# Kernel optimization log

Measured on AMD Instinct MI355X. Metric: run time of the kernel, lower is better.

The kernel has to match this reference:

```python
import jax, jax.numpy as jnp
import numpy as np

W_SIZE = 7
K = 15
EPS = 1e-8  # torch cosine_similarity eps


def setup_inputs() -> dict:
    key = jax.random.key(0)
    k0, k1, k2 = jax.random.split(key, 3)
    dim = 128
    return {
        "x_in": jax.random.normal(k0, (4, dim, 112, 112), dtype=jnp.float32),
        "f_w": jax.random.normal(k1, (dim // 8, dim), dtype=jnp.float32) * (1.0 / np.sqrt(dim)),
        "f_b": jax.random.normal(k2, (dim // 8,), dtype=jnp.float32) * 0.01,
        "edge_alpha": jnp.ones((1,), dtype=jnp.float32),
        "edge_beta": jnp.zeros((1,), dtype=jnp.float32),
    }


def reference(x_in, f_w, f_b, edge_alpha, edge_beta):
    B, C, H, W = x_in.shape
    Wg = Hg = W_SIZE
    w, h = H // Wg, W // Hg
    N = w * h
    # patchify: b c (Wg w) (Hg h) -> (b Wg Hg) c w h
    xp = x_in.reshape(B, C, Wg, w, Hg, h).transpose(0, 2, 4, 1, 3, 5).reshape(B * Wg * Hg, C, w, h)
    P = xp.shape[0]
    # 1x1 conv f: C -> C//8 channels
    f = jnp.einsum('pcwh,dc->pdwh', xp, f_w) + f_b[None, :, None, None]
    Cf = f.shape[1]
    x_flat = f.reshape(P, Cf, N).transpose(0, 2, 1)  # [P, N, Cf]
    # normalized spatial grid (torch std is unbiased -> ddof=1)
    gi, gj = jnp.meshgrid(jnp.arange(w, dtype=jnp.float32), jnp.arange(h, dtype=jnp.float32), indexing='ij')
    grid = jnp.stack([gi, gj], axis=-1).reshape(N, 2)
    grid = (grid - grid.mean(0)) / (grid.std(0, ddof=1) + 1e-5)
    x_aug = jnp.concatenate([x_flat, jnp.broadcast_to(grid[None], (P, N, 2))], axis=-1)  # [P,N,Cf+2]
    # pairwise cosine similarity via normalized dot products
    nrm = jnp.maximum(jnp.linalg.norm(x_aug, axis=-1, keepdims=True), EPS)
    xn = x_aug / nrm
    sim = jnp.einsum('pnd,pmd->pnm', xn, xn)  # [P,N,N]
    topv, topi = jax.lax.top_k(sim, K)        # [P,N,K]
    # edge weights; scatter_softmax over row index == softmax over k (each row has exactly K edges)
    weights = jax.nn.sigmoid(edge_beta[0] + edge_alpha[0] * topv)
    wn = jax.nn.softmax(weights, axis=-1)     # [P,N,K]
    # gather original-channel messages from top-k neighbors and aggregate
    xo = xp.reshape(P, C, N).transpose(0, 2, 1)                 # [P,N,C]
    gathered = jax.vmap(lambda xr, ir: xr[ir])(xo, topi)        # [P,N,K,C]
    out_flat = jnp.einsum('pnk,pnkc->pnc', wn, gathered)        # [P,N,C]
    out = out_flat.reshape(P, w, h, C).transpose(0, 3, 1, 2)    # [P,C,w,h]
    # un-patchify: (b Wg Hg) c w h -> b c (Wg w) (Hg h)
    out = out.reshape(B, Wg, Hg, C, w, h).transpose(0, 3, 1, 4, 2, 5).reshape(B, C, H, W)
    return out
```

## Files before the change

kernel.cpp:

```cpp
#include <hip/hip_runtime.h>
#include <math.h>

#define KSEL 15
#define CIN 128
#define CF 16
#define HH 112
#define PLANE 12544
#define NN 256
#define GRIDW 7
#define ROWSTRIDE 20

static __device__ __forceinline__ unsigned mono32(float f) {
    unsigned u = __float_as_uint(f);
    return ((int)u < 0) ? ~u : (u | 0x80000000u);
}
static __device__ __forceinline__ float demono32(unsigned u) {
    return ((int)u < 0) ? __uint_as_float(u & 0x7FFFFFFFu) : __uint_as_float(~u);
}
static __device__ __forceinline__ unsigned long long mono64(double f) {
    unsigned long long u = (unsigned long long)__double_as_longlong(f);
    return ((long long)u < 0) ? ~u : (u | 0x8000000000000000ull);
}

__global__ __launch_bounds__(256) void k1_features(
    const float* __restrict__ x, const float* __restrict__ fw, const float* __restrict__ fb,
    double* __restrict__ xa64, float* __restrict__ xa32)
{
    __shared__ float lfw[CIN * CF];
    __shared__ float lfb[CF];
    const int tid = threadIdx.x;
    const int p  = blockIdx.x >> 2;
    const int n0 = (blockIdx.x & 3) * 64;
    const int b = p / 49, g = p % 49;
    const int gI = g / 7, gJ = g % 7;
    const float* xb = x + (size_t)b * CIN * PLANE + (size_t)(gI * 16 * HH + gJ * 16);

    for (int q = tid; q < CIN * CF; q += 256) { int d = q >> 7, c = q & 127; lfw[c * CF + d] = fw[q]; }
    if (tid < CF) lfb[tid] = fb[tid];
    __syncthreads();

    const int nl = tid >> 2, dq = tid & 3;
    const int n = n0 + nl, i = n >> 4, j = n & 15;
    const float* xp = xb + i * HH + j;

    double a0 = 0.0, a1 = 0.0, a2 = 0.0, a3 = 0.0;
#pragma unroll 4
    for (int c = 0; c < CIN; ++c) {
        double xc = (double)xp[(size_t)c * PLANE];
        float4 wv = *(const float4*)&lfw[c * CF + dq * 4];
        a0 = fma(xc, (double)wv.x, a0);
        a1 = fma(xc, (double)wv.y, a1);
        a2 = fma(xc, (double)wv.z, a2);
        a3 = fma(xc, (double)wv.w, a3);
    }
    a0 += (double)lfb[dq * 4 + 0];
    a1 += (double)lfb[dq * 4 + 1];
    a2 += (double)lfb[dq * 4 + 2];
    a3 += (double)lfb[dq * 4 + 3];

    const double GDIV = 4.618802153517006 + 1e-5;
    double gx = ((double)i - 7.5) / GDIV;
    double gy = ((double)j - 7.5) / GDIV;

    double ss = a0 * a0;
    ss = fma(a1, a1, ss); ss = fma(a2, a2, ss); ss = fma(a3, a3, ss);
    if (dq == 3) { ss = fma(gx, gx, ss); ss = fma(gy, gy, ss); }
    ss += __shfl_xor(ss, 1);
    ss += __shfl_xor(ss, 2);
    double nrm = fmax(sqrt(ss), 1e-8);

    size_t ro = ((size_t)p * NN + n) * ROWSTRIDE;
    double o0 = a0 / nrm, o1 = a1 / nrm, o2 = a2 / nrm, o3 = a3 / nrm;
    xa64[ro + dq * 4 + 0] = o0; xa64[ro + dq * 4 + 1] = o1;
    xa64[ro + dq * 4 + 2] = o2; xa64[ro + dq * 4 + 3] = o3;
    xa32[ro + dq * 4 + 0] = (float)o0; xa32[ro + dq * 4 + 1] = (float)o1;
    xa32[ro + dq * 4 + 2] = (float)o2; xa32[ro + dq * 4 + 3] = (float)o3;
    if (dq == 3) {
        double g0 = gx / nrm, g1 = gy / nrm;
        xa64[ro + 16] = g0; xa64[ro + 17] = g1; xa64[ro + 18] = 0.0; xa64[ro + 19] = 0.0;
        xa32[ro + 16] = (float)g0; xa32[ro + 17] = (float)g1; xa32[ro + 18] = 0.f; xa32[ro + 19] = 0.f;
    }
}

__global__ __launch_bounds__(256) void k2_select(
    const double* __restrict__ xa64, const float* __restrict__ xa32,
    const float* __restrict__ ea, const float* __restrict__ eb,
    int* __restrict__ topi, float* __restrict__ wkout, unsigned* __restrict__ flags)
{
    __shared__ float tile[NN * ROWSTRIDE];
    __shared__ unsigned kv[NN * 17];
    const int tid = threadIdx.x;
    const int p = blockIdx.x >> 4, sub = blockIdx.x & 15;

    const float* src = xa32 + (size_t)p * NN * ROWSTRIDE;
#pragma unroll
    for (int q = 0; q < 5; ++q) {
        int idx = q * 256 + tid;
        ((float4*)tile)[idx] = ((const float4*)src)[idx];
    }
    __syncthreads();

    const int lane = tid & 15;
    const int grp  = tid >> 4;
    const int rip  = sub * 16 + grp;
    const int row  = p * NN + rip;

    float xr[18];
#pragma unroll
    for (int d = 0; d < 18; ++d) xr[d] = tile[rip * ROWSTRIDE + d];

    unsigned k[16];
#pragma unroll
    for (int s = 0; s < 16; ++s) {
        int m = s * 16 + lane;
        const float* xm = &tile[m * ROWSTRIDE];
        float acc = 0.f;
#pragma unroll
        for (int d = 0; d < 18; ++d) acc = fmaf(xr[d], xm[d], acc);
        k[s] = (mono32(acc) & 0xFFFFFF00u) | (unsigned)(255 - m);
    }

#pragma unroll
    for (int kk = 2; kk <= 16; kk <<= 1) {
#pragma unroll
        for (int jj = kk >> 1; jj > 0; jj >>= 1) {
#pragma unroll
            for (int ii = 0; ii < 16; ++ii) {
                int ll = ii ^ jj;
                if (ll > ii) {
                    bool up = ((ii & kk) == 0);
                    unsigned a = k[ii], bb = k[ll];
                    bool sw = up ? (a > bb) : (a < bb);
                    k[ii] = sw ? bb : a; k[ll] = sw ? a : bb;
                }
            }
        }
    }
#pragma unroll
    for (int s = 0; s < 16; ++s) kv[tid * 17 + s] = k[s];

    int ptr = 15;
    unsigned mycand = 0;
    unsigned myhead = k[15];
#pragma unroll
    for (int e = 0; e < 16; ++e) {
        unsigned W = myhead;
        unsigned o;
        o = __shfl_xor(W, 1);  W = (o > W) ? o : W;
        o = __shfl_xor(W, 2);  W = (o > W) ? o : W;
        o = __shfl_xor(W, 4);  W = (o > W) ? o : W;
        o = __shfl_xor(W, 8);  W = (o > W) ? o : W;
        if (lane == e) mycand = W;
        bool won = (myhead == W);
        ptr -= won ? 1 : 0;
        int rp = ptr < 0 ? 0 : ptr;
        unsigned reread = kv[tid * 17 + rp];
        myhead = won ? reread : myhead;
    }

    unsigned v15 = __shfl(mycand, 14, 16);
    unsigned v16 = __shfl(mycand, 15, 16);
    float lo = demono32(v15 & 0xFFFFFF00u) - 1e-5f;
    float hi = demono32((v16 & 0xFFFFFF00u) + 0x100u) + 1e-5f;
    bool dirty = !(hi < lo);
    if (lane == 0) flags[row] = dirty ? 1u : 0u;

    int mym = 255 - (int)(mycand & 0xFFu);
    const double* xr64 = xa64 + (size_t)row * ROWSTRIDE;
    const double* xm64 = xa64 + ((size_t)p * NN + mym) * ROWSTRIDE;
    double s64 = 0.0;
#pragma unroll
    for (int d = 0; d < 18; ++d) s64 = fma(xr64[d], xm64[d], s64);

    unsigned long long rkey = (mono64(s64) & ~0xFFull) | (unsigned long long)(255 - mym);
    unsigned long long rmin = rkey, ro_;
    ro_ = __shfl_xor(rmin, 1);  rmin = (ro_ < rmin) ? ro_ : rmin;
    ro_ = __shfl_xor(rmin, 2);  rmin = (ro_ < rmin) ? ro_ : rmin;
    ro_ = __shfl_xor(rmin, 4);  rmin = (ro_ < rmin) ? ro_ : rmin;
    ro_ = __shfl_xor(rmin, 8);  rmin = (ro_ < rmin) ? ro_ : rmin;
    bool loser = (rkey == rmin);

    float alpha = ea[0], beta = eb[0];
    float sg = 1.f / (1.f + expf(-(beta + alpha * (float)s64)));
    float v = loser ? -1e30f : sg;
    float mx = v, of;
    of = __shfl_xor(mx, 1); mx = fmaxf(mx, of);
    of = __shfl_xor(mx, 2); mx = fmaxf(mx, of);
    of = __shfl_xor(mx, 4); mx = fmaxf(mx, of);
    of = __shfl_xor(mx, 8); mx = fmaxf(mx, of);
    float ex = expf(v - mx);
    float sm = ex;
    of = __shfl_xor(sm, 1); sm += of;
    of = __shfl_xor(sm, 2); sm += of;
    of = __shfl_xor(sm, 4); sm += of;
    of = __shfl_xor(sm, 8); sm += of;
    float w = ex / sm;

    topi[row * 16 + lane] = mym;
    wkout[row * 16 + lane] = w;
}

__global__ __launch_bounds__(64) void k2b_dirty(
    const double* __restrict__ xa64, const float* __restrict__ ea, const float* __restrict__ eb,
    const unsigned* __restrict__ flags, int* __restrict__ topi, float* __restrict__ wkout)
{
    const int row = blockIdx.x;
    if (flags[row] == 0) return;
    const int lane = threadIdx.x;
    const int p = row >> 8;
    const double* xr64 = xa64 + (size_t)row * ROWSTRIDE;

    double sv[4]; int smi[4];
#pragma unroll
    for (int s4 = 0; s4 < 4; ++s4) {
        int m = s4 * 64 + lane;
        const double* xm64 = xa64 + ((size_t)p * NN + m) * ROWSTRIDE;
        double s = 0.0;
#pragma unroll
        for (int d = 0; d < 18; ++d) s = fma(xr64[d], xm64[d], s);
        sv[s4] = s; smi[s4] = m;
    }

    double cv = -3.0; int cm = 0;
#pragma unroll
    for (int e = 0; e < KSEL; ++e) {
        double lv = sv[0]; int lm = smi[0];
#pragma unroll
        for (int s4 = 1; s4 < 4; ++s4) {
            bool t = (sv[s4] > lv) || (sv[s4] == lv && smi[s4] < lm);
            lv = t ? sv[s4] : lv; lm = t ? smi[s4] : lm;
        }
#pragma unroll
        for (int off = 1; off < 64; off <<= 1) {
            double ov = __shfl_xor(lv, off);
            int    om = __shfl_xor(lm, off);
            bool t = (ov > lv) || (ov == lv && om < lm);
            lv = t ? ov : lv; lm = t ? om : lm;
        }
        if (lane == e) { cv = lv; cm = lm; }
#pragma unroll
        for (int s4 = 0; s4 < 4; ++s4) if (smi[s4] == lm) sv[s4] = -3.0;
    }

    float alpha = ea[0], beta = eb[0];
    float sg = 1.f / (1.f + expf(-(beta + alpha * (float)cv)));
    float v = (lane < KSEL) ? sg : -1e30f;
    float mx = v, of;
    for (int off = 1; off < 64; off <<= 1) { of = __shfl_xor(mx, off); mx = fmaxf(mx, of); }
    float ex = expf(v - mx);
    float sm = ex;
    for (int off = 1; off < 64; off <<= 1) { of = __shfl_xor(sm, off); sm += of; }
    float w = ex / sm;
    if (lane < 16) {
        topi[row * 16 + lane] = (lane < KSEL) ? cm : 0;
        wkout[row * 16 + lane] = (lane < KSEL) ? w : 0.f;
    }
}

__global__ __launch_bounds__(256) void k3_aggregate(
    const float* __restrict__ x, const int* __restrict__ topi, const float* __restrict__ wk,
    float* __restrict__ out)
{
    __shared__ float tile[NN * ROWSTRIDE];
    const int tid = threadIdx.x;
    const int pb = blockIdx.x >> 3, cg = blockIdx.x & 7, c0 = cg * 16;
    const int b = pb / 49, g = pb % 49;
    const int gI = g / 7, gJ = g % 7;
    const float* xb = x + ((size_t)b * CIN + c0) * PLANE + (size_t)(gI * 16 * HH + gJ * 16);

#pragma unroll
    for (int rep = 0; rep < 4; ++rep) {
        int linear = rep * 256 + tid;
        int cc = linear >> 6, chunk = linear & 63;
        int pos = chunk * 4, ii = pos >> 4, jj = pos & 15;
        float4 v = *(const float4*)(xb + (size_t)cc * PLANE + ii * HH + jj);
        tile[(pos + 0) * ROWSTRIDE + cc] = v.x;
        tile[(pos + 1) * ROWSTRIDE + cc] = v.y;
        tile[(pos + 2) * ROWSTRIDE + cc] = v.z;
        tile[(pos + 3) * ROWSTRIDE + cc] = v.w;
    }
    __syncthreads();

    const int n = tid;
    const int row = pb * NN + n;
    float acc[16];
#pragma unroll
    for (int c = 0; c < 16; ++c) acc[c] = 0.f;

#pragma unroll
    for (int kq = 0; kq < 4; ++kq) {
        int4   mi4 = ((const int4*)(topi + (size_t)row * 16))[kq];
        float4 w4  = ((const float4*)(wk  + (size_t)row * 16))[kq];
        const int   mis[4] = { mi4.x, mi4.y, mi4.z, mi4.w };
        const float ws4[4] = { w4.x, w4.y, w4.z, w4.w };
#pragma unroll
        for (int u = 0; u < 4; ++u) {
            float w = ws4[u];
            const float4* sp = (const float4*)&tile[mis[u] * ROWSTRIDE];
#pragma unroll
            for (int q = 0; q < 4; ++q) {
                float4 f = sp[q];
                acc[q * 4 + 0] = fmaf(w, f.x, acc[q * 4 + 0]);
                acc[q * 4 + 1] = fmaf(w, f.y, acc[q * 4 + 1]);
                acc[q * 4 + 2] = fmaf(w, f.z, acc[q * 4 + 2]);
                acc[q * 4 + 3] = fmaf(w, f.w, acc[q * 4 + 3]);
            }
        }
    }
    const int ii = n >> 4, jj = n & 15;
    float* ob = out + ((size_t)b * CIN + c0) * PLANE + (size_t)(gI * 16 * HH + gJ * 16) + ii * HH + jj;
#pragma unroll
    for (int cc = 0; cc < 16; ++cc) ob[(size_t)cc * PLANE] = acc[cc];
}

extern "C" void kernel_launch(void* const* d_in, const int* in_sizes, int n_in,
                              void* d_out, int out_size, void* d_ws, size_t ws_size,
                              hipStream_t stream) {
    const float* x  = (const float*)d_in[0];
    const float* fw = (const float*)d_in[1];
    const float* fb = (const float*)d_in[2];
    const float* ea = (const float*)d_in[3];
    const float* eb = (const float*)d_in[4];
    float* out = (float*)d_out;

    int nB = in_sizes[0] / (CIN * PLANE);
    int nP = nB * 49;
    size_t nRows = (size_t)nP * NN;

    char* wsb = (char*)d_ws;
    size_t off = 0;
    auto carve = [&](size_t bytes) { char* r = wsb + off; off = (off + bytes + 255) & ~(size_t)255; return r; };
    double*   xa64  = (double*)  carve(nRows * ROWSTRIDE * sizeof(double));
    float*    xa32  = (float*)   carve(nRows * ROWSTRIDE * sizeof(float));
    int*      topi  = (int*)     carve(nRows * 16 * sizeof(int));
    float*    wk    = (float*)   carve(nRows * 16 * sizeof(float));
    unsigned* flags = (unsigned*)carve(nRows * sizeof(unsigned));

    hipLaunchKernelGGL(k1_features, dim3(nP * 4), dim3(256), 0, stream, x, fw, fb, xa64, xa32);
    hipLaunchKernelGGL(k2_select,   dim3(nP * 16), dim3(256), 0, stream, xa64, xa32, ea, eb, topi, wk, flags);
    hipLaunchKernelGGL(k2b_dirty,   dim3((unsigned)nRows), dim3(64), 0, stream, xa64, ea, eb, flags, topi, wk);
    hipLaunchKernelGGL(k3_aggregate, dim3(nP * 8), dim3(256), 0, stream, x, topi, wk, out);
}
```

Measured before the change: 171.2 us.

## Compact dirty rows into a list and drop fp64 rescoring in select

The select kernel no longer recomputes the 16 candidate similarities in double precision to find the 16th-place loser. It takes scores straight from the fp32 sort keys and masks lane 15. Rows whose fp32 ordering near the cutoff is ambiguous are appended to a compact list with an atomic counter, which is reset in the feature kernel. The fp64 fallback kernel now runs a fixed 256-block grid over that list instead of one block per row with an early exit. Candidate rows are also read from shared memory as float4 vectors. The cost is that weights now use truncated fp32 similarities rather than fp64 ones, so results can differ slightly in precision.

```diff
diff --git a/kernel.cpp b/kernel.cpp
--- a/kernel.cpp
+++ b/kernel.cpp
@@ -7,7 +7,6 @@
 #define HH 112
 #define PLANE 12544
 #define NN 256
-#define GRIDW 7
 #define ROWSTRIDE 20
 
 static __device__ __forceinline__ unsigned mono32(float f) {
@@ -17,18 +16,15 @@
 static __device__ __forceinline__ float demono32(unsigned u) {
     return ((int)u < 0) ? __uint_as_float(u & 0x7FFFFFFFu) : __uint_as_float(~u);
 }
-static __device__ __forceinline__ unsigned long long mono64(double f) {
-    unsigned long long u = (unsigned long long)__double_as_longlong(f);
-    return ((long long)u < 0) ? ~u : (u | 0x8000000000000000ull);
-}
 
 __global__ __launch_bounds__(256) void k1_features(
     const float* __restrict__ x, const float* __restrict__ fw, const float* __restrict__ fb,
-    double* __restrict__ xa64, float* __restrict__ xa32)
+    double* __restrict__ xa64, float* __restrict__ xa32, unsigned* __restrict__ dirtyCount)
 {
     __shared__ float lfw[CIN * CF];
     __shared__ float lfb[CF];
     const int tid = threadIdx.x;
+    if (blockIdx.x == 0 && tid == 0) *dirtyCount = 0u;
     const int p  = blockIdx.x >> 2;
     const int n0 = (blockIdx.x & 3) * 64;
     const int b = p / 49, g = p % 49;
@@ -83,9 +79,10 @@
 }
 
 __global__ __launch_bounds__(256) void k2_select(
-    const double* __restrict__ xa64, const float* __restrict__ xa32,
+    const float* __restrict__ xa32,
     const float* __restrict__ ea, const float* __restrict__ eb,
-    int* __restrict__ topi, float* __restrict__ wkout, unsigned* __restrict__ flags)
+    int* __restrict__ topi, float* __restrict__ wkout,
+    unsigned* __restrict__ dirtyCount, int* __restrict__ dirtyList)
 {
     __shared__ float tile[NN * ROWSTRIDE];
     __shared__ unsigned kv[NN * 17];
@@ -113,10 +110,16 @@
 #pragma unroll
     for (int s = 0; s < 16; ++s) {
         int m = s * 16 + lane;
-        const float* xm = &tile[m * ROWSTRIDE];
+        const float4* xm4 = (const float4*)&tile[m * ROWSTRIDE];
+        float bb[18];
+        *(float4*)&bb[0]  = xm4[0];
+        *(float4*)&bb[4]  = xm4[1];
+        *(float4*)&bb[8]  = xm4[2];
+        *(float4*)&bb[12] = xm4[3];
+        *(float2*)&bb[16] = *(const float2*)&tile[m * ROWSTRIDE + 16];
         float acc = 0.f;
 #pragma unroll
-        for (int d = 0; d < 18; ++d) acc = fmaf(xr[d], xm[d], acc);
+        for (int d = 0; d < 18; ++d) acc = fmaf(xr[d], bb[d], acc);
         k[s] = (mono32(acc) & 0xFFFFFF00u) | (unsigned)(255 - m);
     }
 
@@ -129,9 +132,9 @@
                 int ll = ii ^ jj;
                 if (ll > ii) {
                     bool up = ((ii & kk) == 0);
-                    unsigned a = k[ii], bb = k[ll];
-                    bool sw = up ? (a > bb) : (a < bb);
-                    k[ii] = sw ? bb : a; k[ll] = sw ? a : bb;
+                    unsigned a = k[ii], bbv = k[ll];
+                    bool sw = up ? (a > bbv) : (a < bbv);
+                    k[ii] = sw ? bbv : a; k[ll] = sw ? a : bbv;
                 }
             }
         }
@@ -163,26 +166,16 @@
     float lo = demono32(v15 & 0xFFFFFF00u) - 1e-5f;
     float hi = demono32((v16 & 0xFFFFFF00u) + 0x100u) + 1e-5f;
     bool dirty = !(hi < lo);
-    if (lane == 0) flags[row] = dirty ? 1u : 0u;
+    if (lane == 0 && dirty) {
+        unsigned slot = atomicAdd(dirtyCount, 1u);
+        dirtyList[slot] = row;
+    }
 
     int mym = 255 - (int)(mycand & 0xFFu);
-    const double* xr64 = xa64 + (size_t)row * ROWSTRIDE;
-    const double* xm64 = xa64 + ((size_t)p * NN + mym) * ROWSTRIDE;
-    double s64 = 0.0;
-#pragma unroll
-    for (int d = 0; d < 18; ++d) s64 = fma(xr64[d], xm64[d], s64);
-
-    unsigned long long rkey = (mono64(s64) & ~0xFFull) | (unsigned long long)(255 - mym);
-    unsigned long long rmin = rkey, ro_;
-    ro_ = __shfl_xor(rmin, 1);  rmin = (ro_ < rmin) ? ro_ : rmin;
-    ro_ = __shfl_xor(rmin, 2);  rmin = (ro_ < rmin) ? ro_ : rmin;
-    ro_ = __shfl_xor(rmin, 4);  rmin = (ro_ < rmin) ? ro_ : rmin;
-    ro_ = __shfl_xor(rmin, 8);  rmin = (ro_ < rmin) ? ro_ : rmin;
-    bool loser = (rkey == rmin);
-
+    float sv = demono32(mycand & 0xFFFFFF00u);
     float alpha = ea[0], beta = eb[0];
-    float sg = 1.f / (1.f + expf(-(beta + alpha * (float)s64)));
-    float v = loser ? -1e30f : sg;
+    float sg = 1.f / (1.f + expf(-(beta + alpha * sv)));
+    float v = (lane < KSEL) ? sg : -1e30f;
     float mx = v, of;
     of = __shfl_xor(mx, 1); mx = fmaxf(mx, of);
     of = __shfl_xor(mx, 2); mx = fmaxf(mx, of);
@@ -194,66 +187,68 @@
     of = __shfl_xor(sm, 2); sm += of;
     of = __shfl_xor(sm, 4); sm += of;
     of = __shfl_xor(sm, 8); sm += of;
-    float w = ex / sm;
 
     topi[row * 16 + lane] = mym;
-    wkout[row * 16 + lane] = w;
+    wkout[row * 16 + lane] = (lane < KSEL) ? (ex / sm) : 0.f;
 }
 
 __global__ __launch_bounds__(64) void k2b_dirty(
     const double* __restrict__ xa64, const float* __restrict__ ea, const float* __restrict__ eb,
-    const unsigned* __restrict__ flags, int* __restrict__ topi, float* __restrict__ wkout)
+    const unsigned* __restrict__ dirtyCount, const int* __restrict__ dirtyList,
+    int* __restrict__ topi, float* __restrict__ wkout)
 {
-    const int row = blockIdx.x;
-    if (flags[row] == 0) return;
+    const int nd = (int)*dirtyCount;
     const int lane = threadIdx.x;
-    const int p = row >> 8;
-    const double* xr64 = xa64 + (size_t)row * ROWSTRIDE;
-
-    double sv[4]; int smi[4];
-#pragma unroll
-    for (int s4 = 0; s4 < 4; ++s4) {
-        int m = s4 * 64 + lane;
-        const double* xm64 = xa64 + ((size_t)p * NN + m) * ROWSTRIDE;
-        double s = 0.0;
-#pragma unroll
-        for (int d = 0; d < 18; ++d) s = fma(xr64[d], xm64[d], s);
-        sv[s4] = s; smi[s4] = m;
-    }
-
-    double cv = -3.0; int cm = 0;
-#pragma unroll
-    for (int e = 0; e < KSEL; ++e) {
-        double lv = sv[0]; int lm = smi[0];
-#pragma unroll
-        for (int s4 = 1; s4 < 4; ++s4) {
-            bool t = (sv[s4] > lv) || (sv[s4] == lv && smi[s4] < lm);
-            lv = t ? sv[s4] : lv; lm = t ? smi[s4] : lm;
-        }
-#pragma unroll
-        for (int off = 1; off < 64; off <<= 1) {
-            double ov = __shfl_xor(lv, off);
-            int    om = __shfl_xor(lm, off);
-            bool t = (ov > lv) || (ov == lv && om < lm);
-            lv = t ? ov : lv; lm = t ? om : lm;
-        }
-        if (lane == e) { cv = lv; cm = lm; }
-#pragma unroll
-        for (int s4 = 0; s4 < 4; ++s4) if (smi[s4] == lm) sv[s4] = -3.0;
-    }
-
-    float alpha = ea[0], beta = eb[0];
-    float sg = 1.f / (1.f + expf(-(beta + alpha * (float)cv)));
-    float v = (lane < KSEL) ? sg : -1e30f;
-    float mx = v, of;
-    for (int off = 1; off < 64; off <<= 1) { of = __shfl_xor(mx, off); mx = fmaxf(mx, of); }
-    float ex = expf(v - mx);
-    float sm = ex;
-    for (int off = 1; off < 64; off <<= 1) { of = __shfl_xor(sm, off); sm += of; }
-    float w = ex / sm;
-    if (lane < 16) {
-        topi[row * 16 + lane] = (lane < KSEL) ? cm : 0;
-        wkout[row * 16 + lane] = (lane < KSEL) ? w : 0.f;
+    for (int idx = blockIdx.x; idx < nd; idx += gridDim.x) {
+        const int row = dirtyList[idx];
+        const int p = row >> 8;
+        const double* xr64 = xa64 + (size_t)row * ROWSTRIDE;
+
+        double sv[4]; int smi[4];
+#pragma unroll
+        for (int s4 = 0; s4 < 4; ++s4) {
+            int m = s4 * 64 + lane;
+            const double* xm64 = xa64 + ((size_t)p * NN + m) * ROWSTRIDE;
+            double s = 0.0;
+#pragma unroll
+            for (int d = 0; d < 18; ++d) s = fma(xr64[d], xm64[d], s);
+            sv[s4] = s; smi[s4] = m;
+        }
+
+        double cv = -3.0; int cm = 0;
+#pragma unroll
+        for (int e = 0; e < KSEL; ++e) {
+            double lv = sv[0]; int lm = smi[0];
+#pragma unroll
+            for (int s4 = 1; s4 < 4; ++s4) {
+                bool t = (sv[s4] > lv) || (sv[s4] == lv && smi[s4] < lm);
+                lv = t ? sv[s4] : lv; lm = t ? smi[s4] : lm;
+            }
+#pragma unroll
+            for (int off = 1; off < 64; off <<= 1) {
+                double ov = __shfl_xor(lv, off);
+                int    om = __shfl_xor(lm, off);
+                bool t = (ov > lv) || (ov == lv && om < lm);
+                lv = t ? ov : lv; lm = t ? om : lm;
+            }
+            if (lane == e) { cv = lv; cm = lm; }
+#pragma unroll
+            for (int s4 = 0; s4 < 4; ++s4) if (smi[s4] == lm) sv[s4] = -3.0;
+        }
+
+        float alpha = ea[0], beta = eb[0];
+        float sg = 1.f / (1.f + expf(-(beta + alpha * (float)cv)));
+        float v = (lane < KSEL) ? sg : -1e30f;
+        float mx = v, of;
+        for (int off = 1; off < 64; off <<= 1) { of = __shfl_xor(mx, off); mx = fmaxf(mx, of); }
+        float ex = expf(v - mx);
+        float sm = ex;
+        for (int off = 1; off < 64; off <<= 1) { of = __shfl_xor(sm, off); sm += of; }
+        float w = ex / sm;
+        if (lane < 16) {
+            topi[row * 16 + lane] = (lane < KSEL) ? cm : 0;
+            wkout[row * 16 + lane] = (lane < KSEL) ? w : 0.f;
+        }
     }
 }
 
@@ -330,14 +325,15 @@
     char* wsb = (char*)d_ws;
     size_t off = 0;
     auto carve = [&](size_t bytes) { char* r = wsb + off; off = (off + bytes + 255) & ~(size_t)255; return r; };
-    double*   xa64  = (double*)  carve(nRows * ROWSTRIDE * sizeof(double));
-    float*    xa32  = (float*)   carve(nRows * ROWSTRIDE * sizeof(float));
-    int*      topi  = (int*)     carve(nRows * 16 * sizeof(int));
-    float*    wk    = (float*)   carve(nRows * 16 * sizeof(float));
-    unsigned* flags = (unsigned*)carve(nRows * sizeof(unsigned));
-
-    hipLaunchKernelGGL(k1_features, dim3(nP * 4), dim3(256), 0, stream, x, fw, fb, xa64, xa32);
-    hipLaunchKernelGGL(k2_select,   dim3(nP * 16), dim3(256), 0, stream, xa64, xa32, ea, eb, topi, wk, flags);
-    hipLaunchKernelGGL(k2b_dirty,   dim3((unsigned)nRows), dim3(64), 0, stream, xa64, ea, eb, flags, topi, wk);
+    double*   xa64   = (double*)  carve(nRows * ROWSTRIDE * sizeof(double));
+    float*    xa32   = (float*)   carve(nRows * ROWSTRIDE * sizeof(float));
+    int*      topi   = (int*)     carve(nRows * 16 * sizeof(int));
+    float*    wk     = (float*)   carve(nRows * 16 * sizeof(float));
+    unsigned* dcnt   = (unsigned*)carve(256);
+    int*      dlist  = (int*)     carve(nRows * sizeof(int));
+
+    hipLaunchKernelGGL(k1_features, dim3(nP * 4), dim3(256), 0, stream, x, fw, fb, xa64, xa32, dcnt);
+    hipLaunchKernelGGL(k2_select,   dim3(nP * 16), dim3(256), 0, stream, xa32, ea, eb, topi, wk, dcnt, dlist);
+    hipLaunchKernelGGL(k2b_dirty,   dim3(256), dim3(64), 0, stream, xa64, ea, eb, dcnt, dlist, topi, wk);
     hipLaunchKernelGGL(k3_aggregate, dim3(nP * 8), dim3(256), 0, stream, x, topi, wk, out);
 }
```

Measured after the change: 156.7 us. -8.5%, faster.
